# Kernel optimization log

Hardware: AMD Instinct MI355X
Metric: run time of the kernel (lower is better)

The kernel has to match this reference:

```python
import jax, jax.numpy as jnp
import numpy as np

IN_CH = 256
INTER_CH = 128
B, H, W = 8, 64, 64


def setup_inputs() -> dict:
    key = jax.random.key(0)
    ks = jax.random.split(key, 9)
    s_in = 1.0 / np.sqrt(IN_CH)
    s_int = 1.0 / np.sqrt(INTER_CH)
    return {
        "x": jax.random.normal(ks[0], (B, IN_CH, H, W), dtype=jnp.float32),
        "g_w": jax.random.normal(ks[1], (INTER_CH, IN_CH), dtype=jnp.float32) * s_in,
        "g_b": jax.random.normal(ks[2], (INTER_CH,), dtype=jnp.float32) * s_in,
        "theta_w": jax.random.normal(ks[3], (INTER_CH, IN_CH), dtype=jnp.float32) * s_in,
        "theta_b": jax.random.normal(ks[4], (INTER_CH,), dtype=jnp.float32) * s_in,
        "phi_w": jax.random.normal(ks[5], (INTER_CH, IN_CH), dtype=jnp.float32) * s_in,
        "phi_b": jax.random.normal(ks[6], (INTER_CH,), dtype=jnp.float32) * s_in,
        "W_w": jax.random.normal(ks[7], (IN_CH, INTER_CH), dtype=jnp.float32) * s_int,
        "W_b": jax.random.normal(ks[8], (IN_CH,), dtype=jnp.float32) * s_int,
    }


def _conv1x1(x, w, b):
    # x: [B,C,H,W], w: [O,C], b: [O] -> [B,O,H,W]
    return jnp.einsum("bchw,oc->bohw", x, w) + b[None, :, None, None]


def reference(x, g_w, g_b, theta_w, theta_b, phi_w, phi_b, W_w, W_b):
    b, c, h, w = x.shape
    n = h * w
    ic = g_w.shape[0]
    # 1x1 conv projections, flattened over spatial positions
    g_x = _conv1x1(x, g_w, g_b).reshape(b, ic, n).transpose(0, 2, 1)      # [B,N,ic]
    theta_x = _conv1x1(x, theta_w, theta_b).reshape(b, ic, n).transpose(0, 2, 1)  # [B,N,ic]
    phi_x = _conv1x1(x, phi_w, phi_b).reshape(b, ic, n)                   # [B,ic,N]
    f = jnp.einsum("bnc,bcm->bnm", theta_x, phi_x)                        # [B,N,N]
    # NOTE: original uses F.softmax(f, dim=1) -> normalize over axis 1 (rows)
    f_div_C = jax.nn.softmax(f, axis=1)
    y = jnp.einsum("bnm,bmc->bnc", f_div_C, g_x)                          # [B,N,ic]
    y = y.transpose(0, 2, 1).reshape(b, ic, h, w)                         # [B,ic,H,W]
    W_y = _conv1x1(y, W_w, W_b)                                           # [B,C,H,W]
    return W_y + x
```

## Files before the change

kernel.cpp:

```cpp
#include <hip/hip_runtime.h>
#include <hip/hip_bf16.h>


#define IC   128
#define CIN  256
#define NPOS 4096
#define NB   8

typedef _Float16 f16;
typedef __attribute__((ext_vector_type(8))) _Float16 f16x8;
typedef __attribute__((ext_vector_type(4))) _Float16 f16x4;
typedef __attribute__((ext_vector_type(4))) float f32x4;
typedef __attribute__((ext_vector_type(4))) float fvec4;

#define MFMA16(a, b, c) __builtin_amdgcn_mfma_f32_16x16x32_f16((a), (b), (c), 0, 0, 0)

__global__ __launch_bounds__(256) void k_prep_w(
    const float* __restrict__ gw, const float* __restrict__ tw, const float* __restrict__ pw,
    const float* __restrict__ Ww, f16* __restrict__ wAll, f16* __restrict__ Wc)
{
    const int idx = (blockIdx.x * 256 + threadIdx.x) * 4;
    if (idx < 384 * 256) {
        const int row = idx >> 8, col = idx & 255;
        const float* src = (row < 128) ? (gw + row * 256)
                         : (row < 256) ? (tw + (row - 128) * 256)
                                       : (pw + (row - 256) * 256);
        fvec4 v = *reinterpret_cast<const fvec4*>(src + col);
        f16x4 o = { (f16)v[0], (f16)v[1], (f16)v[2], (f16)v[3] };
        *reinterpret_cast<f16x4*>(wAll + idx) = o;
    } else {
        const int j = idx - 384 * 256;
        fvec4 v = *reinterpret_cast<const fvec4*>(Ww + j);
        f16x4 o = { (f16)v[0], (f16)v[1], (f16)v[2], (f16)v[3] };
        *reinterpret_cast<f16x4*>(Wc + j) = o;
    }
}

__global__ __launch_bounds__(256) void k_split_x(
    const float* __restrict__ x, f16* __restrict__ xT)
{
    __shared__ float tile[64][65];
    const int b  = blockIdx.z;
    const int c0 = blockIdx.y * 64;
    const int n0 = blockIdx.x * 64;
    const int t  = threadIdx.x;
    {
        const int cc = t >> 4, nn = (t & 15) * 4;
        const float* src = x + ((size_t)b * CIN + c0) * NPOS + n0;
#pragma unroll
        for (int p = 0; p < 4; ++p) {
            fvec4 v = *reinterpret_cast<const fvec4*>(src + (size_t)(cc + p * 16) * NPOS + nn);
            tile[cc + p * 16][nn + 0] = v[0];
            tile[cc + p * 16][nn + 1] = v[1];
            tile[cc + p * 16][nn + 2] = v[2];
            tile[cc + p * 16][nn + 3] = v[3];
        }
    }
    __syncthreads();
    {
        const int c4 = (t & 15) * 4, nr = t >> 4;
#pragma unroll
        for (int p = 0; p < 4; ++p) {
            const int n = nr + p * 16;
            f16x4 o = { (f16)tile[c4 + 0][n], (f16)tile[c4 + 1][n],
                        (f16)tile[c4 + 2][n], (f16)tile[c4 + 3][n] };
            *reinterpret_cast<f16x4*>(xT + ((size_t)b * NPOS + n0 + n) * CIN + c0 + c4) = o;
        }
    }
}

__global__ __launch_bounds__(256) void k_proj(
    const f16* __restrict__ xT, const f16* __restrict__ wAll,
    const float* __restrict__ gb, const float* __restrict__ tb, const float* __restrict__ pb,
    f16* __restrict__ th, f16* __restrict__ ph, f16* __restrict__ gT)
{
    const int w    = threadIdx.x >> 6;
    const int lane = threadIdx.x & 63;
    const int lrow = lane & 15;
    const int kg   = lane >> 4;
    const int b    = blockIdx.z;
    const int c0   = blockIdx.y * 64;
    const int n0   = blockIdx.x * 256 + w * 64;

    const f16* X = xT + (size_t)b * NPOS * CIN;

    f32x4 acc[4][4] = {};
#pragma unroll
    for (int ks = 0; ks < 8; ++ks) {
        const int k = ks * 32 + kg * 8;
        f16x8 a[4], bv[4];
#pragma unroll
        for (int i = 0; i < 4; ++i) {
            a[i]  = *reinterpret_cast<const f16x8*>(wAll + (size_t)(c0 + i * 16 + lrow) * CIN + k);
            bv[i] = *reinterpret_cast<const f16x8*>(X + (size_t)(n0 + i * 16 + lrow) * CIN + k);
        }
#pragma unroll
        for (int i = 0; i < 4; ++i)
#pragma unroll
            for (int j = 0; j < 4; ++j)
                acc[i][j] = MFMA16(a[i], bv[j], acc[i][j]);
    }
    const int set = c0 >> 7;
    if (set == 0) {
#pragma unroll
        for (int i = 0; i < 4; ++i) {
            const int c = c0 + i * 16 + kg * 4;
#pragma unroll
            for (int j = 0; j < 4; ++j) {
                const int n = n0 + j * 16 + lrow;
#pragma unroll
                for (int r = 0; r < 4; ++r)
                    gT[((size_t)b * IC + c + r) * NPOS + n] = (f16)(acc[i][j][r] + gb[c + r]);
            }
        }
    } else {
        const float* Bi = (set == 1) ? tb : pb;
        f16* dst = (set == 1) ? th : ph;
        const int cl0 = (c0 & 127);
#pragma unroll
        for (int i = 0; i < 4; ++i) {
            const int c = cl0 + i * 16 + kg * 4;
#pragma unroll
            for (int j = 0; j < 4; ++j) {
                const int n = n0 + j * 16 + lrow;
                f16x4 o = { (f16)(acc[i][j][0] + Bi[c + 0]), (f16)(acc[i][j][1] + Bi[c + 1]),
                            (f16)(acc[i][j][2] + Bi[c + 2]), (f16)(acc[i][j][3] + Bi[c + 3]) };
                *reinterpret_cast<f16x4*>(dst + ((size_t)b * NPOS + n) * IC + c) = o;
            }
        }
    }
}

__global__ __launch_bounds__(256, 4) void k_gemm1(
    const f16* __restrict__ th, const f16* __restrict__ ph,
    f16* __restrict__ Ep, float* __restrict__ lmax, float* __restrict__ lsum, int b0)
{
    __shared__ f16 Alds[128 * 64];
    __shared__ f16 Blds[128 * 64];
    const int t    = threadIdx.x;
    const int w    = t >> 6;
    const int lane = t & 63;
    const int lrow = lane & 15;
    const int kg   = lane >> 4;
    const int wm   = w & 1;
    const int wn   = w >> 1;
    const int bi   = blockIdx.x >> 10;
    const int rest = blockIdx.x & 1023;
    const int mblk = rest & 31;
    const int nblk = rest >> 5;

    const f16* Ag = ph + (size_t)(b0 + bi) * NPOS * IC + (size_t)(mblk * 128) * IC;
    const f16* Bg = th + (size_t)(b0 + bi) * NPOS * IC + (size_t)(nblk * 128) * IC;

    const int trow = t >> 3;
    const int tc   = t & 7;

    f32x4 acc[4][4] = {};
#pragma unroll
    for (int h = 0; h < 2; ++h) {
        if (h) __syncthreads();
#pragma unroll
        for (int it = 0; it < 4; ++it) {
            const int row = trow + it * 32;
            const int cs  = tc ^ (row & 7);
            *reinterpret_cast<f16x8*>(&Alds[row * 64 + cs * 8]) =
                *reinterpret_cast<const f16x8*>(Ag + (size_t)row * IC + h * 64 + tc * 8);
            *reinterpret_cast<f16x8*>(&Blds[row * 64 + cs * 8]) =
                *reinterpret_cast<const f16x8*>(Bg + (size_t)row * IC + h * 64 + tc * 8);
        }
        __syncthreads();
#pragma unroll
        for (int ks = 0; ks < 2; ++ks) {
            f16x8 a[4], bv[4];
#pragma unroll
            for (int i = 0; i < 4; ++i) {
                const int mr = wm * 64 + i * 16 + lrow;
                const int cs = (ks * 4 + kg) ^ (mr & 7);
                a[i] = *reinterpret_cast<const f16x8*>(&Alds[mr * 64 + cs * 8]);
            }
#pragma unroll
            for (int j = 0; j < 4; ++j) {
                const int nr = wn * 64 + j * 16 + lrow;
                const int cs = (ks * 4 + kg) ^ (nr & 7);
                bv[j] = *reinterpret_cast<const f16x8*>(&Blds[nr * 64 + cs * 8]);
            }
#pragma unroll
            for (int i = 0; i < 4; ++i)
#pragma unroll
                for (int j = 0; j < 4; ++j)
                    acc[i][j] = MFMA16(a[i], bv[j], acc[i][j]);
        }
    }

    const int m0 = mblk * 128 + wm * 64;
    const int n0 = nblk * 128 + wn * 64;
    f16* eb = Ep + (size_t)bi * NPOS * NPOS;
    const float L2E = 1.4426950408889634f;

    f32x4 cm[4], ncml[4];
#pragma unroll
    for (int i = 0; i < 4; ++i)
#pragma unroll
        for (int r = 0; r < 4; ++r) {
            float c = fmaxf(fmaxf(acc[i][0][r], acc[i][1][r]),
                            fmaxf(acc[i][2][r], acc[i][3][r]));
            c = fmaxf(c, __shfl_xor(c, 1));
            c = fmaxf(c, __shfl_xor(c, 2));
            c = fmaxf(c, __shfl_xor(c, 4));
            c = fmaxf(c, __shfl_xor(c, 8));
            cm[i][r] = c;
            ncml[i][r] = -c * L2E;
        }

    f32x4 s[4] = {};
#pragma unroll
    for (int j = 0; j < 4; ++j) {
        f16* rowp = eb + (size_t)(n0 + j * 16 + lrow) * NPOS + m0 + kg * 4;
#pragma unroll
        for (int i = 0; i < 4; ++i) {
            f16x4 ev;
#pragma unroll
            for (int r = 0; r < 4; ++r) {
                float e = exp2f(__builtin_fmaf(acc[i][j][r], L2E, ncml[i][r]));
                s[i][r] += e;
                ev[r] = (f16)e;
            }
            *reinterpret_cast<f16x4*>(rowp + i * 16) = ev;
        }
    }

    const int rowblk = nblk * 2 + wn;
#pragma unroll
    for (int i = 0; i < 4; ++i)
#pragma unroll
        for (int r = 0; r < 4; ++r) {
            float ss = s[i][r];
            ss += __shfl_xor(ss, 1);
            ss += __shfl_xor(ss, 2);
            ss += __shfl_xor(ss, 4);
            ss += __shfl_xor(ss, 8);
            if (lrow == 0) {
                const size_t off = ((size_t)bi * 64 + rowblk) * NPOS + m0 + i * 16 + kg * 4 + r;
                lmax[off] = cm[i][r];
                lsum[off] = ss;
            }
        }
}

__global__ __launch_bounds__(256) void k_prep(
    const float* __restrict__ lmax, const float* __restrict__ lsum,
    const f16* __restrict__ gT, f16* __restrict__ sca, f16* __restrict__ gs, int b0)
{
    const int bi = blockIdx.y;
    const int m  = blockIdx.x * 256 + threadIdx.x;
    const float* lm = lmax + (size_t)bi * 64 * NPOS;
    const float* ls = lsum + (size_t)bi * 64 * NPOS;
    float cm = -3.0e38f;
#pragma unroll 8
    for (int rb = 0; rb < 64; ++rb)
        cm = fmaxf(cm, lm[(size_t)rb * NPOS + m]);
    float s = 0.f;
    f16* scab = sca + (size_t)bi * 64 * NPOS;
#pragma unroll 8
    for (int rb = 0; rb < 64; ++rb) {
        float e = __expf(lm[(size_t)rb * NPOS + m] - cm);
        s += e * ls[(size_t)rb * NPOS + m];
        scab[(size_t)rb * NPOS + m] = (f16)e;
    }
    const float rc = 1.0f / s;
    const f16* gb = gT + (size_t)(b0 + bi) * IC * NPOS;
    f16* gsb = gs + (size_t)bi * IC * NPOS;
#pragma unroll 8
    for (int c = 0; c < IC; ++c)
        gsb[(size_t)c * NPOS + m] = (f16)((float)gb[(size_t)c * NPOS + m] * rc);
}

__global__ __launch_bounds__(256, 4) void k_gemm2(
    const f16* __restrict__ Ep, const f16* __restrict__ sca,
    const f16* __restrict__ gs, f16* __restrict__ partial)
{
    __shared__ f16 Elds[128 * 64];
    __shared__ f16 Glds[128 * 64];
    const int t    = threadIdx.x;
    const int w    = t >> 6;
    const int lane = t & 63;
    const int lrow = lane & 15;
    const int kg   = lane >> 4;
    const int wc   = w & 1;
    const int wn   = w >> 1;
    const int bi   = blockIdx.x >> 7;
    const int rest = blockIdx.x & 127;
    const int kc   = rest & 3;
    const int nblk = rest >> 2;

    const f16* Eg  = Ep + (size_t)bi * NPOS * NPOS + (size_t)(nblk * 128) * NPOS + kc * 1024;
    const f16* Gg  = gs + (size_t)bi * IC * NPOS + kc * 1024;
    const int  rb  = nblk * 2 + wn;
    const f16* srow = sca + ((size_t)bi * 64 + rb) * NPOS + kc * 1024;

    const int trow = t >> 3;
    const int tc   = t & 7;

    f32x4 acc[4][4] = {};
    for (int sc = 0; sc < 16; ++sc) {
        if (sc) __syncthreads();
#pragma unroll
        for (int it = 0; it < 4; ++it) {
            const int row = trow + it * 32;
            const int cs  = tc ^ (row & 7);
            *reinterpret_cast<f16x8*>(&Elds[row * 64 + cs * 8]) =
                *reinterpret_cast<const f16x8*>(Eg + (size_t)row * NPOS + sc * 64 + tc * 8);
            *reinterpret_cast<f16x8*>(&Glds[row * 64 + cs * 8]) =
                *reinterpret_cast<const f16x8*>(Gg + (size_t)row * NPOS + sc * 64 + tc * 8);
        }
        __syncthreads();

#pragma unroll
        for (int ks = 0; ks < 2; ++ks) {
            f16x8 sv = *reinterpret_cast<const f16x8*>(srow + sc * 64 + ks * 32 + kg * 8);
            f16x8 a[4], ev[4];
#pragma unroll
            for (int i = 0; i < 4; ++i) {
                const int cr = wc * 64 + i * 16 + lrow;
                const int cs = (ks * 4 + kg) ^ (cr & 7);
                a[i] = *reinterpret_cast<const f16x8*>(&Glds[cr * 64 + cs * 8]);
            }
#pragma unroll
            for (int j = 0; j < 4; ++j) {
                const int nr = wn * 64 + j * 16 + lrow;
                const int cs = (ks * 4 + kg) ^ (nr & 7);
                ev[j] = *reinterpret_cast<const f16x8*>(&Elds[nr * 64 + cs * 8]) * sv;
            }
#pragma unroll
            for (int i = 0; i < 4; ++i)
#pragma unroll
                for (int j = 0; j < 4; ++j)
                    acc[i][j] = MFMA16(a[i], ev[j], acc[i][j]);
        }
    }

    f16* pb = partial + ((size_t)bi * 4 + kc) * NPOS * IC;
    const int n0 = nblk * 128 + wn * 64;
    const int c0 = wc * 64;
#pragma unroll
    for (int j = 0; j < 4; ++j) {
        f16* rowp = pb + (size_t)(n0 + j * 16 + lrow) * IC + c0 + kg * 4;
#pragma unroll
        for (int i = 0; i < 4; ++i) {
            f16x4 o = { (f16)acc[i][j][0], (f16)acc[i][j][1],
                        (f16)acc[i][j][2], (f16)acc[i][j][3] };
            *reinterpret_cast<f16x4*>(rowp + i * 16) = o;
        }
    }
}

__global__ __launch_bounds__(256) void k_reduce(
    const f16* __restrict__ partial, f16* __restrict__ yT, int b0)
{
    const int bi  = blockIdx.y;
    const int idx = blockIdx.x * 256 + threadIdx.x;
    const f16x8* p = reinterpret_cast<const f16x8*>(partial + (size_t)bi * 4 * NPOS * IC);
    float s[8] = {};
#pragma unroll
    for (int kc = 0; kc < 4; ++kc) {
        f16x8 v = p[(size_t)kc * (NPOS * IC / 8) + idx];
#pragma unroll
        for (int k = 0; k < 8; ++k)
            s[k] += (float)v[k];
    }
    f16x8 o;
#pragma unroll
    for (int k = 0; k < 8; ++k)
        o[k] = (f16)s[k];
    *reinterpret_cast<f16x8*>(yT + (size_t)(b0 + bi) * NPOS * IC + (size_t)idx * 8) = o;
}

__global__ __launch_bounds__(256) void k_conv(
    const float* __restrict__ x, const f16* __restrict__ Wc, const float* __restrict__ Wb,
    const f16* __restrict__ yT, float* __restrict__ out)
{
    const int w    = threadIdx.x >> 6;
    const int lane = threadIdx.x & 63;
    const int lrow = lane & 15;
    const int kg   = lane >> 4;
    const int gwid = blockIdx.x * 4 + w;
    const int ob   = gwid & 3;
    const int nb   = (gwid >> 2) & 63;
    const int b    = gwid >> 8;
    const int o0   = ob * 64;
    const int n0   = nb * 64;

    const f16* Y = yT + (size_t)b * NPOS * IC;
    f32x4 acc[4][4] = {};
#pragma unroll
    for (int ks = 0; ks < 4; ++ks) {
        const int k = ks * 32 + kg * 8;
        f16x8 a[4], bv[4];
#pragma unroll
        for (int i = 0; i < 4; ++i) {
            a[i]  = *reinterpret_cast<const f16x8*>(Wc + (size_t)(o0 + i * 16 + lrow) * IC + k);
            bv[i] = *reinterpret_cast<const f16x8*>(Y + (size_t)(n0 + i * 16 + lrow) * IC + k);
        }
#pragma unroll
        for (int i = 0; i < 4; ++i)
#pragma unroll
            for (int j = 0; j < 4; ++j)
                acc[i][j] = MFMA16(a[i], bv[j], acc[i][j]);
    }
#pragma unroll
    for (int i = 0; i < 4; ++i) {
        const int o = o0 + i * 16 + kg * 4;
#pragma unroll
        for (int j = 0; j < 4; ++j) {
            const int n = n0 + j * 16 + lrow;
#pragma unroll
            for (int r = 0; r < 4; ++r) {
                const size_t off = ((size_t)b * CIN + o + r) * NPOS + n;
                out[off] = acc[i][j][r] + x[off] + Wb[o + r];
            }
        }
    }
}

extern "C" void kernel_launch(void* const* d_in, const int* in_sizes, int n_in,
                              void* d_out, int out_size, void* d_ws, size_t ws_size,
                              hipStream_t stream)
{
    const float* x  = (const float*)d_in[0];
    const float* gw = (const float*)d_in[1];
    const float* gb = (const float*)d_in[2];
    const float* tw = (const float*)d_in[3];
    const float* tb = (const float*)d_in[4];
    const float* pw = (const float*)d_in[5];
    const float* pb = (const float*)d_in[6];
    const float* Ww = (const float*)d_in[7];
    const float* Wb = (const float*)d_in[8];
    float* out = (float*)d_out;

    char* ws = (char*)d_ws;
    size_t off = 0;
    auto alloc = [&](size_t bytes) -> char* {
        char* p = ws + off;
        off += (bytes + 255) & ~(size_t)255;
        return p;
    };
    f16* xT   = (f16*)alloc((size_t)NB * NPOS * CIN * 2);
    f16* wAll = (f16*)alloc((size_t)384 * 256 * 2);
    f16* Wc   = (f16*)alloc((size_t)CIN * IC * 2);
    f16* th   = (f16*)alloc((size_t)NB * NPOS * IC * 2);
    f16* ph   = (f16*)alloc((size_t)NB * NPOS * IC * 2);
    f16* gT   = (f16*)alloc((size_t)NB * NPOS * IC * 2);
    f16* Ep   = (f16*)alloc((size_t)4 * NPOS * NPOS * 2);
    float* lmax = (float*)alloc((size_t)4 * 64 * NPOS * 4);
    float* lsum = (float*)alloc((size_t)4 * 64 * NPOS * 4);
    f16* sca  = (f16*)alloc((size_t)4 * 64 * NPOS * 2);
    f16* gs   = (f16*)alloc((size_t)4 * IC * NPOS * 2);
    f16* partial = (f16*)alloc((size_t)4 * 4 * NPOS * IC * 2);
    f16* yT   = (f16*)alloc((size_t)NB * NPOS * IC * 2);

    k_prep_w<<<128, 256, 0, stream>>>(gw, tw, pw, Ww, wAll, Wc);
    k_split_x<<<dim3(64, 4, 8), 256, 0, stream>>>(x, xT);
    k_proj<<<dim3(16, 6, 8), 256, 0, stream>>>(xT, wAll, gb, tb, pb, th, ph, gT);

    for (int b0 = 0; b0 < NB; b0 += 4) {
        k_gemm1<<<4096, 256, 0, stream>>>(th, ph, Ep, lmax, lsum, b0);
        k_prep<<<dim3(16, 4), 256, 0, stream>>>(lmax, lsum, gT, sca, gs, b0);
        k_gemm2<<<512, 256, 0, stream>>>(Ep, sca, gs, partial);
        k_reduce<<<dim3(256, 4), 256, 0, stream>>>(partial, yT, b0);
    }
    k_conv<<<dim3(512), 256, 0, stream>>>(x, Wc, Wb, yT, out);
}
```

Measured before the change: 343.0 us.

## Double-buffer LDS and prefetch global tiles into registers in both GEMM kernels

The score GEMM now loads the second K-half into registers while the first half is being computed. The second GEMM switches to double-buffered LDS with register prefetch of the next K-chunk, so one barrier per iteration replaces two. Both changes aim to hide global-load latency behind MFMA work. In exchange, the second GEMM uses twice the LDS and its launch bound drops to 2 blocks per CU, which can cut occupancy.

```diff
diff --git a/kernel.cpp b/kernel.cpp
--- a/kernel.cpp
+++ b/kernel.cpp
@@ -155,41 +155,79 @@
     const int trow = t >> 3;
     const int tc   = t & 7;
 
+    f16x8 pa[4], pb[4];
+#pragma unroll
+    for (int it = 0; it < 4; ++it) {
+        const int row = trow + it * 32;
+        pa[it] = *reinterpret_cast<const f16x8*>(Ag + (size_t)row * IC + tc * 8);
+        pb[it] = *reinterpret_cast<const f16x8*>(Bg + (size_t)row * IC + tc * 8);
+    }
+#pragma unroll
+    for (int it = 0; it < 4; ++it) {
+        const int row = trow + it * 32;
+        const int cs  = tc ^ (row & 7);
+        *reinterpret_cast<f16x8*>(&Alds[row * 64 + cs * 8]) = pa[it];
+        *reinterpret_cast<f16x8*>(&Blds[row * 64 + cs * 8]) = pb[it];
+    }
+#pragma unroll
+    for (int it = 0; it < 4; ++it) {
+        const int row = trow + it * 32;
+        pa[it] = *reinterpret_cast<const f16x8*>(Ag + (size_t)row * IC + 64 + tc * 8);
+        pb[it] = *reinterpret_cast<const f16x8*>(Bg + (size_t)row * IC + 64 + tc * 8);
+    }
+    __syncthreads();
+
     f32x4 acc[4][4] = {};
 #pragma unroll
-    for (int h = 0; h < 2; ++h) {
-        if (h) __syncthreads();
-#pragma unroll
-        for (int it = 0; it < 4; ++it) {
-            const int row = trow + it * 32;
-            const int cs  = tc ^ (row & 7);
-            *reinterpret_cast<f16x8*>(&Alds[row * 64 + cs * 8]) =
-                *reinterpret_cast<const f16x8*>(Ag + (size_t)row * IC + h * 64 + tc * 8);
-            *reinterpret_cast<f16x8*>(&Blds[row * 64 + cs * 8]) =
-                *reinterpret_cast<const f16x8*>(Bg + (size_t)row * IC + h * 64 + tc * 8);
-        }
-        __syncthreads();
-#pragma unroll
-        for (int ks = 0; ks < 2; ++ks) {
-            f16x8 a[4], bv[4];
-#pragma unroll
-            for (int i = 0; i < 4; ++i) {
-                const int mr = wm * 64 + i * 16 + lrow;
-                const int cs = (ks * 4 + kg) ^ (mr & 7);
-                a[i] = *reinterpret_cast<const f16x8*>(&Alds[mr * 64 + cs * 8]);
-            }
-#pragma unroll
-            for (int j = 0; j < 4; ++j) {
-                const int nr = wn * 64 + j * 16 + lrow;
-                const int cs = (ks * 4 + kg) ^ (nr & 7);
-                bv[j] = *reinterpret_cast<const f16x8*>(&Blds[nr * 64 + cs * 8]);
-            }
-#pragma unroll
-            for (int i = 0; i < 4; ++i)
-#pragma unroll
-                for (int j = 0; j < 4; ++j)
-                    acc[i][j] = MFMA16(a[i], bv[j], acc[i][j]);
-        }
+    for (int ks = 0; ks < 2; ++ks) {
+        f16x8 a[4], bv[4];
+#pragma unroll
+        for (int i = 0; i < 4; ++i) {
+            const int mr = wm * 64 + i * 16 + lrow;
+            const int cs = (ks * 4 + kg) ^ (mr & 7);
+            a[i] = *reinterpret_cast<const f16x8*>(&Alds[mr * 64 + cs * 8]);
+        }
+#pragma unroll
+        for (int j = 0; j < 4; ++j) {
+            const int nr = wn * 64 + j * 16 + lrow;
+            const int cs = (ks * 4 + kg) ^ (nr & 7);
+            bv[j] = *reinterpret_cast<const f16x8*>(&Blds[nr * 64 + cs * 8]);
+        }
+#pragma unroll
+        for (int i = 0; i < 4; ++i)
+#pragma unroll
+            for (int j = 0; j < 4; ++j)
+                acc[i][j] = MFMA16(a[i], bv[j], acc[i][j]);
+    }
+    __syncthreads();
+#pragma unroll
+    for (int it = 0; it < 4; ++it) {
+        const int row = trow + it * 32;
+        const int cs  = tc ^ (row & 7);
+        *reinterpret_cast<f16x8*>(&Alds[row * 64 + cs * 8]) = pa[it];
+        *reinterpret_cast<f16x8*>(&Blds[row * 64 + cs * 8]) = pb[it];
+    }
+    __syncthreads();
+#pragma unroll
+    for (int ks = 0; ks < 2; ++ks) {
+        f16x8 a[4], bv[4];
+#pragma unroll
+        for (int i = 0; i < 4; ++i) {
+            const int mr = wm * 64 + i * 16 + lrow;
+            const int cs = (ks * 4 + kg) ^ (mr & 7);
+            a[i] = *reinterpret_cast<const f16x8*>(&Alds[mr * 64 + cs * 8]);
+        }
+#pragma unroll
+        for (int j = 0; j < 4; ++j) {
+            const int nr = wn * 64 + j * 16 + lrow;
+            const int cs = (ks * 4 + kg) ^ (nr & 7);
+            bv[j] = *reinterpret_cast<const f16x8*>(&Blds[nr * 64 + cs * 8]);
+        }
+#pragma unroll
+        for (int i = 0; i < 4; ++i)
+#pragma unroll
+            for (int j = 0; j < 4; ++j)
+                acc[i][j] = MFMA16(a[i], bv[j], acc[i][j]);
     }
 
     const int m0 = mblk * 128 + wm * 64;
@@ -275,12 +313,12 @@
         gsb[(size_t)c * NPOS + m] = (f16)((float)gb[(size_t)c * NPOS + m] * rc);
 }
 
-__global__ __launch_bounds__(256, 4) void k_gemm2(
+__global__ __launch_bounds__(256, 2) void k_gemm2(
     const f16* __restrict__ Ep, const f16* __restrict__ sca,
     const f16* __restrict__ gs, f16* __restrict__ partial)
 {
-    __shared__ f16 Elds[128 * 64];
-    __shared__ f16 Glds[128 * 64];
+    __shared__ f16 Elds[2][128 * 64];
+    __shared__ f16 Glds[2][128 * 64];
     const int t    = threadIdx.x;
     const int w    = t >> 6;
     const int lane = t & 63;
@@ -301,17 +339,31 @@
     const int trow = t >> 3;
     const int tc   = t & 7;
 
+    f16x8 pe[4], pg[4];
+#pragma unroll
+    for (int it = 0; it < 4; ++it) {
+        const int row = trow + it * 32;
+        pe[it] = *reinterpret_cast<const f16x8*>(Eg + (size_t)row * NPOS + tc * 8);
+        pg[it] = *reinterpret_cast<const f16x8*>(Gg + (size_t)row * NPOS + tc * 8);
+    }
+
     f32x4 acc[4][4] = {};
     for (int sc = 0; sc < 16; ++sc) {
-        if (sc) __syncthreads();
+        const int cur = sc & 1;
 #pragma unroll
         for (int it = 0; it < 4; ++it) {
             const int row = trow + it * 32;
             const int cs  = tc ^ (row & 7);
-            *reinterpret_cast<f16x8*>(&Elds[row * 64 + cs * 8]) =
-                *reinterpret_cast<const f16x8*>(Eg + (size_t)row * NPOS + sc * 64 + tc * 8);
-            *reinterpret_cast<f16x8*>(&Glds[row * 64 + cs * 8]) =
-                *reinterpret_cast<const f16x8*>(Gg + (size_t)row * NPOS + sc * 64 + tc * 8);
+            *reinterpret_cast<f16x8*>(&Elds[cur][row * 64 + cs * 8]) = pe[it];
+            *reinterpret_cast<f16x8*>(&Glds[cur][row * 64 + cs * 8]) = pg[it];
+        }
+        if (sc < 15) {
+#pragma unroll
+            for (int it = 0; it < 4; ++it) {
+                const int row = trow + it * 32;
+                pe[it] = *reinterpret_cast<const f16x8*>(Eg + (size_t)row * NPOS + (sc + 1) * 64 + tc * 8);
+                pg[it] = *reinterpret_cast<const f16x8*>(Gg + (size_t)row * NPOS + (sc + 1) * 64 + tc * 8);
+            }
         }
         __syncthreads();
 
@@ -323,13 +375,13 @@
             for (int i = 0; i < 4; ++i) {
                 const int cr = wc * 64 + i * 16 + lrow;
                 const int cs = (ks * 4 + kg) ^ (cr & 7);
-                a[i] = *reinterpret_cast<const f16x8*>(&Glds[cr * 64 + cs * 8]);
+                a[i] = *reinterpret_cast<const f16x8*>(&Glds[cur][cr * 64 + cs * 8]);
             }
 #pragma unroll
             for (int j = 0; j < 4; ++j) {
                 const int nr = wn * 64 + j * 16 + lrow;
                 const int cs = (ks * 4 + kg) ^ (nr & 7);
-                ev[j] = *reinterpret_cast<const f16x8*>(&Elds[nr * 64 + cs * 8]) * sv;
+                ev[j] = *reinterpret_cast<const f16x8*>(&Elds[cur][nr * 64 + cs * 8]) * sv;
             }
 #pragma unroll
             for (int i = 0; i < 4; ++i)
```

After: 328.1 us. -4.3%, faster.

## Double-buffer gemm2 LDS with register prefetch, swizzle block order, use fast exp2

Applied to the files above, without the earlier changes.

k_gemm2 now keeps two LDS buffers and prefetches the next K-slice into registers while the current slice is computed. This removes one barrier per iteration and overlaps global loads with MFMA work, at the cost of twice the LDS and a lower occupancy hint (launch bounds 4 to 2). Both GEMM kernels remap blockIdx so that consecutive blocks are spread across batches, which is meant to improve cache and channel locality. The exp calls in gemm1 and prep switch to the hardware exp2 intrinsic, and gemm1 packs its f16 output with cvt_pkrtz, which rounds toward zero instead of to nearest.

```diff
diff --git a/kernel.cpp b/kernel.cpp
--- a/kernel.cpp
+++ b/kernel.cpp
@@ -12,8 +12,10 @@
 typedef __attribute__((ext_vector_type(4))) _Float16 f16x4;
 typedef __attribute__((ext_vector_type(4))) float f32x4;
 typedef __attribute__((ext_vector_type(4))) float fvec4;
+typedef __attribute__((ext_vector_type(2))) unsigned int u32x2;
 
 #define MFMA16(a, b, c) __builtin_amdgcn_mfma_f32_16x16x32_f16((a), (b), (c), 0, 0, 0)
+#define EXP2(x) __builtin_amdgcn_exp2f(x)
 
 __global__ __launch_bounds__(256) void k_prep_w(
     const float* __restrict__ gw, const float* __restrict__ tw, const float* __restrict__ pw,
@@ -144,8 +146,9 @@
     const int kg   = lane >> 4;
     const int wm   = w & 1;
     const int wn   = w >> 1;
-    const int bi   = blockIdx.x >> 10;
-    const int rest = blockIdx.x & 1023;
+    const int swz  = (blockIdx.x & 7) * 512 + (blockIdx.x >> 3);
+    const int bi   = swz >> 10;
+    const int rest = swz & 1023;
     const int mblk = rest & 31;
     const int nblk = rest >> 5;
 
@@ -218,14 +221,14 @@
         f16* rowp = eb + (size_t)(n0 + j * 16 + lrow) * NPOS + m0 + kg * 4;
 #pragma unroll
         for (int i = 0; i < 4; ++i) {
-            f16x4 ev;
-#pragma unroll
-            for (int r = 0; r < 4; ++r) {
-                float e = exp2f(__builtin_fmaf(acc[i][j][r], L2E, ncml[i][r]));
-                s[i][r] += e;
-                ev[r] = (f16)e;
-            }
-            *reinterpret_cast<f16x4*>(rowp + i * 16) = ev;
+            float e0 = EXP2(__builtin_fmaf(acc[i][j][0], L2E, ncml[i][0]));
+            float e1 = EXP2(__builtin_fmaf(acc[i][j][1], L2E, ncml[i][1]));
+            float e2 = EXP2(__builtin_fmaf(acc[i][j][2], L2E, ncml[i][2]));
+            float e3 = EXP2(__builtin_fmaf(acc[i][j][3], L2E, ncml[i][3]));
+            s[i][0] += e0; s[i][1] += e1; s[i][2] += e2; s[i][3] += e3;
+            u32x2 o = { __builtin_bit_cast(unsigned int, __builtin_amdgcn_cvt_pkrtz(e0, e1)),
+                        __builtin_bit_cast(unsigned int, __builtin_amdgcn_cvt_pkrtz(e2, e3)) };
+            *reinterpret_cast<u32x2*>(rowp + i * 16) = o;
         }
     }
 
@@ -251,6 +254,7 @@
     const float* __restrict__ lmax, const float* __restrict__ lsum,
     const f16* __restrict__ gT, f16* __restrict__ sca, f16* __restrict__ gs, int b0)
 {
+    const float L2E = 1.4426950408889634f;
     const int bi = blockIdx.y;
     const int m  = blockIdx.x * 256 + threadIdx.x;
     const float* lm = lmax + (size_t)bi * 64 * NPOS;
@@ -263,7 +267,7 @@
     f16* scab = sca + (size_t)bi * 64 * NPOS;
 #pragma unroll 8
     for (int rb = 0; rb < 64; ++rb) {
-        float e = __expf(lm[(size_t)rb * NPOS + m] - cm);
+        float e = EXP2((lm[(size_t)rb * NPOS + m] - cm) * L2E);
         s += e * ls[(size_t)rb * NPOS + m];
         scab[(size_t)rb * NPOS + m] = (f16)e;
     }
@@ -275,12 +279,12 @@
         gsb[(size_t)c * NPOS + m] = (f16)((float)gb[(size_t)c * NPOS + m] * rc);
 }
 
-__global__ __launch_bounds__(256, 4) void k_gemm2(
+__global__ __launch_bounds__(256, 2) void k_gemm2(
     const f16* __restrict__ Ep, const f16* __restrict__ sca,
     const f16* __restrict__ gs, f16* __restrict__ partial)
 {
-    __shared__ f16 Elds[128 * 64];
-    __shared__ f16 Glds[128 * 64];
+    __shared__ f16 Elds[2][128 * 64];
+    __shared__ f16 Glds[2][128 * 64];
     const int t    = threadIdx.x;
     const int w    = t >> 6;
     const int lane = t & 63;
@@ -288,8 +292,9 @@
     const int kg   = lane >> 4;
     const int wc   = w & 1;
     const int wn   = w >> 1;
-    const int bi   = blockIdx.x >> 7;
-    const int rest = blockIdx.x & 127;
+    const int swz  = (blockIdx.x & 7) * 64 + (blockIdx.x >> 3);
+    const int bi   = swz >> 7;
+    const int rest = swz & 127;
     const int kc   = rest & 3;
     const int nblk = rest >> 2;
 
@@ -301,17 +306,31 @@
     const int trow = t >> 3;
     const int tc   = t & 7;
 
+    f16x8 pe[4], pg[4];
+#pragma unroll
+    for (int it = 0; it < 4; ++it) {
+        const int row = trow + it * 32;
+        pe[it] = *reinterpret_cast<const f16x8*>(Eg + (size_t)row * NPOS + tc * 8);
+        pg[it] = *reinterpret_cast<const f16x8*>(Gg + (size_t)row * NPOS + tc * 8);
+    }
+
     f32x4 acc[4][4] = {};
     for (int sc = 0; sc < 16; ++sc) {
-        if (sc) __syncthreads();
+        const int cur = sc & 1;
 #pragma unroll
         for (int it = 0; it < 4; ++it) {
             const int row = trow + it * 32;
             const int cs  = tc ^ (row & 7);
-            *reinterpret_cast<f16x8*>(&Elds[row * 64 + cs * 8]) =
-                *reinterpret_cast<const f16x8*>(Eg + (size_t)row * NPOS + sc * 64 + tc * 8);
-            *reinterpret_cast<f16x8*>(&Glds[row * 64 + cs * 8]) =
-                *reinterpret_cast<const f16x8*>(Gg + (size_t)row * NPOS + sc * 64 + tc * 8);
+            *reinterpret_cast<f16x8*>(&Elds[cur][row * 64 + cs * 8]) = pe[it];
+            *reinterpret_cast<f16x8*>(&Glds[cur][row * 64 + cs * 8]) = pg[it];
+        }
+        if (sc < 15) {
+#pragma unroll
+            for (int it = 0; it < 4; ++it) {
+                const int row = trow + it * 32;
+                pe[it] = *reinterpret_cast<const f16x8*>(Eg + (size_t)row * NPOS + (sc + 1) * 64 + tc * 8);
+                pg[it] = *reinterpret_cast<const f16x8*>(Gg + (size_t)row * NPOS + (sc + 1) * 64 + tc * 8);
+            }
         }
         __syncthreads();
 
@@ -323,13 +342,13 @@
             for (int i = 0; i < 4; ++i) {
                 const int cr = wc * 64 + i * 16 + lrow;
                 const int cs = (ks * 4 + kg) ^ (cr & 7);
-                a[i] = *reinterpret_cast<const f16x8*>(&Glds[cr * 64 + cs * 8]);
+                a[i] = *reinterpret_cast<const f16x8*>(&Glds[cur][cr * 64 + cs * 8]);
             }
 #pragma unroll
             for (int j = 0; j < 4; ++j) {
                 const int nr = wn * 64 + j * 16 + lrow;
                 const int cs = (ks * 4 + kg) ^ (nr & 7);
-                ev[j] = *reinterpret_cast<const f16x8*>(&Elds[nr * 64 + cs * 8]) * sv;
+                ev[j] = *reinterpret_cast<const f16x8*>(&Elds[cur][nr * 64 + cs * 8]) * sv;
             }
 #pragma unroll
             for (int i = 0; i < 4; ++i)
```

Result: faster. 332.9 us (median of 2 runs) (-2.9%).
